# Optimization experiments

Measured on AMD Instinct MI355X. Metric: run time of the kernel, lower is better.

The kernel has to match this reference:

```python
import jax, jax.numpy as jnp
import numpy as np

W_BIT, OUT_F, IN_F, K = 4, 4096, 4096, 16
B, S = 4, 2048


def setup_inputs() -> dict:
    key = jax.random.key(0)
    k1, k2, k3, k4 = jax.random.split(key, 4)
    x = jax.random.normal(k1, (B, S, IN_F), dtype=jnp.float16)
    # bit-packed signs: 8 signs per byte, stored as int32 in [0, 256)
    qweight = jax.random.randint(k2, (W_BIT, OUT_F * IN_F // 8), 0, 256, dtype=jnp.int32)
    u = jax.random.normal(k3, (W_BIT, OUT_F, K), dtype=jnp.float16) * jnp.float16(0.1)
    vt = jax.random.normal(k4, (W_BIT, K, IN_F), dtype=jnp.float16) * jnp.float16(0.1)
    return {"x": x, "qweight": qweight, "u": u, "vt": vt}


def _unpack_sign(qweight, out_f, in_f, dtype):
    # [w_bit, N/8] packed bytes -> [w_bit, out_f, in_f] signs in {-1, +1}
    bits = (qweight[:, :, None] >> jnp.arange(8, dtype=qweight.dtype)) & 1
    sign = (2 * bits - 1).reshape(qweight.shape[0], out_f, in_f)
    return sign.astype(dtype)


def reference(x, qweight, u, vt):
    w_bit, out_f, _ = u.shape
    in_f = vt.shape[2]
    sign = _unpack_sign(qweight, out_f, in_f, u.dtype)          # [w_bit, out, in]
    lowrank = jnp.einsum('bok,bki->boi', u, vt)                  # per-bit u @ vt
    w = jnp.sum(sign * lowrank, axis=0)                          # [out, in]
    return x @ w.T                                               # [B, S, out]
```

## Files before the change

kernel.cpp:

```cpp
#include <hip/hip_runtime.h>
#include <stdint.h>


#define W_BITS 4
#define OUT_F  4096
#define IN_F   4096
#define K_RANK 16
#define M_TOT  8192
#define QW_PER_BIT (OUT_F * IN_F / 8)

typedef __attribute__((ext_vector_type(8))) short bf16x8;
typedef __attribute__((ext_vector_type(4))) float f32x4;

__device__ __forceinline__ unsigned short f2bf(float f) {
  union { float f; unsigned int u; } c; c.f = f;
  unsigned int r = c.u + 0x7fffu + ((c.u >> 16) & 1u);
  return (unsigned short)(r >> 16);
}

__global__ __launch_bounds__(256) void convert_x(
    const float* __restrict__ X, unsigned short* __restrict__ Xb, int n8)
{
  const int stride = gridDim.x * blockDim.x;
  for (int i = blockIdx.x * blockDim.x + threadIdx.x; i < n8; i += stride) {
    const f32x4 a = *reinterpret_cast<const f32x4*>(X + (size_t)i * 8);
    const f32x4 b = *reinterpret_cast<const f32x4*>(X + (size_t)i * 8 + 4);
    unsigned short o8[8] = {f2bf(a[0]), f2bf(a[1]), f2bf(a[2]), f2bf(a[3]),
                            f2bf(b[0]), f2bf(b[1]), f2bf(b[2]), f2bf(b[3])};
    *reinterpret_cast<uint4*>(Xb + (size_t)i * 8) = *reinterpret_cast<const uint4*>(o8);
  }
}

#define TO 4

__global__ __launch_bounds__(256) void build_w(
    const int*   __restrict__ qw,
    const float* __restrict__ u,
    const float* __restrict__ vt,
    unsigned short* __restrict__ w)
{
  const int tid = blockIdx.x * 256 + threadIdx.x;
  const int ig  = tid & 511;
  const int i0  = ig << 3;
  const int ob  = (tid >> 9) << 2;

  float acc[TO][8];
  #pragma unroll
  for (int t = 0; t < TO; ++t)
    #pragma unroll
    for (int ii = 0; ii < 8; ++ii) acc[t][ii] = 0.0f;

  #pragma unroll
  for (int bit = 0; bit < W_BITS; ++bit) {
    float lr[TO][8];
    #pragma unroll
    for (int t = 0; t < TO; ++t)
      #pragma unroll
      for (int ii = 0; ii < 8; ++ii) lr[t][ii] = 0.0f;

    const float* vbase = vt + (size_t)(bit * K_RANK) * IN_F + i0;
    const float* ubase = u + (size_t)(bit * OUT_F + ob) * K_RANK;

    #pragma unroll
    for (int k = 0; k < K_RANK; ++k) {
      const f32x4 v0 = *reinterpret_cast<const f32x4*>(vbase + (size_t)k * IN_F);
      const f32x4 v1 = *reinterpret_cast<const f32x4*>(vbase + (size_t)k * IN_F + 4);
      float vf[8] = {v0[0], v0[1], v0[2], v0[3], v1[0], v1[1], v1[2], v1[3]};
      #pragma unroll
      for (int t = 0; t < TO; ++t) {
        const float uk = ubase[t * K_RANK + k];
        #pragma unroll
        for (int ii = 0; ii < 8; ++ii) lr[t][ii] += uk * vf[ii];
      }
    }

    #pragma unroll
    for (int t = 0; t < TO; ++t) {
      const int q = qw[(size_t)bit * QW_PER_BIT + (size_t)(ob + t) * (IN_F / 8) + ig];
      #pragma unroll
      for (int ii = 0; ii < 8; ++ii)
        acc[t][ii] += ((q >> ii) & 1) ? lr[t][ii] : -lr[t][ii];
    }
  }

  #pragma unroll
  for (int t = 0; t < TO; ++t) {
    unsigned short o8[8];
    #pragma unroll
    for (int ii = 0; ii < 8; ++ii) o8[ii] = f2bf(acc[t][ii]);
    *reinterpret_cast<uint4*>(w + (size_t)(ob + t) * IN_F + i0) =
        *reinterpret_cast<const uint4*>(o8);
  }
}

__device__ __forceinline__ void gll16(unsigned short* lds, const unsigned short* g) {
  __builtin_amdgcn_global_load_lds(
      (const __attribute__((address_space(1))) unsigned int*)g,
      (__attribute__((address_space(3))) unsigned int*)lds,
      16, 0, 0);
}

__global__ __launch_bounds__(512, 2) void gemm_256(
    const unsigned short* __restrict__ X,
    const unsigned short* __restrict__ W,
    float* __restrict__ out)
{
  __shared__ __align__(16) unsigned short Al[2][256][64];
  __shared__ __align__(16) unsigned short Bl[2][256][64];

  const int bid = blockIdx.x;
  const int swz = (bid & 7) * 64 + (bid >> 3);
  const int bm = swz >> 4;
  const int bn = swz & 15;

  const int tid  = threadIdx.x;
  const int lane = tid & 63;
  const int wid  = tid >> 6;
  const int wm   = wid >> 2;
  const int wn   = wid & 3;

  const int sr = tid >> 3;
  const int sc = (((tid & 7) ^ (sr & 7)) << 3);

  const unsigned short* Abase = X + (size_t)(bm * 256 + sr) * IN_F + sc;
  const unsigned short* Bbase = W + (size_t)(bn * 256 + sr) * IN_F + sc;
  unsigned short* Alt = &Al[0][0][0] + tid * 8;
  unsigned short* Blt = &Bl[0][0][0] + tid * 8;

  const int fr  = lane & 15;
  const int sw0 = (((lane >> 4) ^ (fr & 7)) << 3);
  const int aRow = (wm * 16 + fr) * 64;
  const int bRow = (wn * 16 + fr) * 64;
  const unsigned short* Ar = &Al[0][0][0];
  const unsigned short* Br = &Bl[0][0][0];

  f32x4 acc[8][4];
  #pragma unroll
  for (int f = 0; f < 8; ++f)
    #pragma unroll
    for (int g = 0; g < 4; ++g)
      acc[f][g] = (f32x4){0.f, 0.f, 0.f, 0.f};

#define STAGE(buf, h, tn_) do {                                                        \
    const unsigned short* gs_ = ((h) < 2 ? Abase : Bbase)                              \
        + (size_t)(((h) & 1) * 128) * IN_F + (size_t)(tn_) * 64;                       \
    unsigned short* ld_ = ((h) < 2 ? Alt : Blt) + (buf) * 16384 + ((h) & 1) * 8192;    \
    gll16(ld_, gs_);                                                                   \
    gll16(ld_ + 4096, gs_ + (size_t)64 * IN_F);                                        \
  } while (0)

#define WAITBAR() do {                                                                 \
    asm volatile("s_waitcnt vmcnt(4)" ::: "memory");                                   \
    __builtin_amdgcn_s_barrier();                                                      \
    __builtin_amdgcn_sched_barrier(0);                                                 \
  } while (0)

#define LGKMW(n_) do {                                                                 \
    asm volatile("s_waitcnt lgkmcnt(" #n_ ")" ::: "memory");                           \
    __builtin_amdgcn_sched_barrier(0);                                                 \
  } while (0)

#define SB() __builtin_amdgcn_sched_barrier(0)

#define ENDPH() do {                                                                   \
    __builtin_amdgcn_sched_barrier(0);                                                 \
    __builtin_amdgcn_s_barrier();                                                      \
  } while (0)

#define RD_A(base_, mh_, f_, ks_)                                                      \
    aF[f_][ks_] = *reinterpret_cast<const bf16x8*>(                                    \
        Ar + (base_) + ((mh_) * 4 + (f_)) * 2048 + aRow + (((ks_) * 32) ^ sw0))

#define RD_B(dst_, base_, nh_, g_, ks_)                                                \
    dst_[g_][ks_] = *reinterpret_cast<const bf16x8*>(                                  \
        Br + (base_) + ((nh_) * 2 + (g_)) * 4096 + bRow + (((ks_) * 32) ^ sw0))

#define MF(mh_, nh_, f_, g_, ks_, bsrc_)                                               \
    acc[(mh_) * 4 + (f_)][(nh_) * 2 + (g_)] = __builtin_amdgcn_mfma_f32_16x16x32_bf16( \
        aF[f_][ks_], bsrc_[g_][ks_], acc[(mh_) * 4 + (f_)][(nh_) * 2 + (g_)], 0, 0, 0)

#define MF4(mh_, nh_, f_, bsrc_) do {                                                  \
    MF(mh_, nh_, f_, 0, 0, bsrc_); MF(mh_, nh_, f_, 0, 1, bsrc_);                      \
    MF(mh_, nh_, f_, 1, 0, bsrc_); MF(mh_, nh_, f_, 1, 1, bsrc_); } while (0)

#define KTILE(P_, Q_, CC_, OO_, tn_) do {                                              \
    const int cb_ = (CC_) * 16384, ob_ = (OO_) * 16384;                                \
                       \
    STAGE(OO_, 2, tn_);                                                                \
    WAITBAR();                                                                         \
    LGKMW(0);                                                                          \
    __builtin_amdgcn_s_setprio(1);                                                     \
    RD_B(Q_, cb_, 1, 0, 0); SB(); MF4(0, 0, 0, P_); SB();                              \
    RD_B(Q_, cb_, 1, 0, 1); SB(); MF4(0, 0, 1, P_); SB();                              \
    RD_B(Q_, cb_, 1, 1, 0); SB(); MF4(0, 0, 2, P_); SB();                              \
    RD_B(Q_, cb_, 1, 1, 1); SB(); MF4(0, 0, 3, P_);                                    \
    __builtin_amdgcn_s_setprio(0);                                                     \
    ENDPH();                                                                           \
                        \
    STAGE(OO_, 0, tn_);                                                                \
    WAITBAR();                                                                         \
    LGKMW(0);                                                                          \
    __builtin_amdgcn_s_setprio(1);                                                     \
    MF4(0, 1, 0, Q_); SB(); RD_A(cb_, 1, 0, 0); RD_A(cb_, 1, 0, 1); SB();              \
    MF4(0, 1, 1, Q_); SB(); RD_A(cb_, 1, 1, 0); RD_A(cb_, 1, 1, 1); SB();              \
    MF4(0, 1, 2, Q_); SB(); RD_A(cb_, 1, 2, 0); RD_A(cb_, 1, 2, 1); SB();              \
    MF4(0, 1, 3, Q_); SB(); RD_A(cb_, 1, 3, 0); RD_A(cb_, 1, 3, 1);                    \
    __builtin_amdgcn_s_setprio(0);                                                     \
    ENDPH();                                                                           \
                \
    STAGE(OO_, 3, tn_);                                                                \
    WAITBAR();                                                                         \
    LGKMW(0);                                                                          \
    __builtin_amdgcn_s_setprio(1);                                                     \
    MF4(1, 1, 0, Q_); MF4(1, 1, 1, Q_); MF4(1, 1, 2, Q_); MF4(1, 1, 3, Q_);            \
    __builtin_amdgcn_s_setprio(0);                                                     \
    SB();                                                                              \
    RD_B(Q_, ob_, 0, 0, 0); RD_B(Q_, ob_, 0, 0, 1);                                    \
    RD_B(Q_, ob_, 0, 1, 0); RD_B(Q_, ob_, 0, 1, 1);                                    \
    ENDPH();                                                                           \
                  \
    STAGE(OO_, 1, tn_);                                                                \
    WAITBAR();                                                                         \
    LGKMW(4);                                                                          \
    __builtin_amdgcn_s_setprio(1);                                                     \
    MF4(1, 0, 0, P_); SB(); RD_A(ob_, 0, 0, 0); RD_A(ob_, 0, 0, 1); SB();              \
    MF4(1, 0, 1, P_); SB(); RD_A(ob_, 0, 1, 0); RD_A(ob_, 0, 1, 1); SB();              \
    MF4(1, 0, 2, P_); SB(); RD_A(ob_, 0, 2, 0); RD_A(ob_, 0, 2, 1); SB();              \
    MF4(1, 0, 3, P_); SB(); RD_A(ob_, 0, 3, 0); RD_A(ob_, 0, 3, 1);                    \
    __builtin_amdgcn_s_setprio(0);                                                     \
    ENDPH();                                                                           \
  } while (0)

  STAGE(0, 0, 0);
  STAGE(0, 2, 0);
  STAGE(0, 3, 0);
  STAGE(0, 1, 0);
  asm volatile("s_waitcnt vmcnt(4)" ::: "memory");
  __builtin_amdgcn_s_barrier();
  __builtin_amdgcn_sched_barrier(0);

  bf16x8 aF[4][2], bF0[2][2], bF1[2][2];
  RD_A(0, 0, 0, 0); RD_A(0, 0, 0, 1);
  RD_A(0, 0, 1, 0); RD_A(0, 0, 1, 1);
  RD_A(0, 0, 2, 0); RD_A(0, 0, 2, 1);
  RD_A(0, 0, 3, 0); RD_A(0, 0, 3, 1);
  RD_B(bF0, 0, 0, 0, 0); RD_B(bF0, 0, 0, 0, 1);
  RD_B(bF0, 0, 0, 1, 0); RD_B(bF0, 0, 0, 1, 1);

  #pragma unroll 1
  for (int Th = 0; Th < 32; ++Th) {
    const int T0 = 2 * Th;
    const int tnA = T0 + 1;
    const int tnB = (T0 + 2 < 64) ? T0 + 2 : 63;
    KTILE(bF0, bF1, 0, 1, tnA);
    KTILE(bF1, bF0, 1, 0, tnB);
  }

  asm volatile("s_waitcnt vmcnt(0) lgkmcnt(0)" ::: "memory");

  const int rsub = (lane >> 4) << 2;
  #pragma unroll
  for (int f = 0; f < 8; ++f) {
    const int row = bm * 256 + (f * 2 + wm) * 16 + rsub;
    #pragma unroll
    for (int g = 0; g < 4; ++g) {
      const int col = bn * 256 + (g * 4 + wn) * 16 + (lane & 15);
      float* op = out + (size_t)row * OUT_F + col;
      #pragma unroll
      for (int j = 0; j < 4; ++j) op[(size_t)j * OUT_F] = acc[f][g][j];
    }
  }
#undef STAGE
#undef WAITBAR
#undef LGKMW
#undef SB
#undef ENDPH
#undef RD_A
#undef RD_B
#undef MF
#undef MF4
#undef KTILE
}

#define BM 128
#define BN 128
#define BK 32

__device__ __forceinline__ uint4 cvt8(f32x4 a, f32x4 b) {
  unsigned short o8[8] = {f2bf(a[0]), f2bf(a[1]), f2bf(a[2]), f2bf(a[3]),
                          f2bf(b[0]), f2bf(b[1]), f2bf(b[2]), f2bf(b[3])};
  return *reinterpret_cast<const uint4*>(o8);
}

__global__ __launch_bounds__(256) void gemm_f32stage(
    const float* __restrict__ X,
    const unsigned short* __restrict__ W,
    float* __restrict__ out)
{
  __shared__ __align__(16) unsigned short As[BM * BK];
  __shared__ __align__(16) unsigned short Bs[BN * BK];

  const int nbn = OUT_F / BN;
  const int cpx = (M_TOT / BM) * nbn / 8;
  const int bid = blockIdx.x;
  const int swz = (bid & 7) * cpx + (bid >> 3);
  const int bm = swz / nbn;
  const int bn = swz % nbn;

  const int tid  = threadIdx.x;
  const int lane = tid & 63;
  const int wid  = tid >> 6;
  const int wm   = wid >> 1;
  const int wn   = wid & 1;
  const int srow = tid >> 2;
  const int scol = (tid & 3) << 3;

  const float*          Ag = X + (size_t)(bm * BM + srow) * IN_F + scol;
  const unsigned short* Bg = W + (size_t)(bn * BN + srow) * IN_F + scol;

  const int fr = lane & 15;
  const int fk = (lane >> 4) << 3;

  f32x4 acc[4][4];
  #pragma unroll
  for (int m = 0; m < 4; ++m)
    #pragma unroll
    for (int n = 0; n < 4; ++n)
      acc[m][n] = (f32x4){0.f, 0.f, 0.f, 0.f};

  for (int k0 = 0; k0 < IN_F; k0 += BK) {
    const f32x4 a0a = *reinterpret_cast<const f32x4*>(Ag + k0);
    const f32x4 a0b = *reinterpret_cast<const f32x4*>(Ag + k0 + 4);
    const f32x4 a1a = *reinterpret_cast<const f32x4*>(Ag + (size_t)64 * IN_F + k0);
    const f32x4 a1b = *reinterpret_cast<const f32x4*>(Ag + (size_t)64 * IN_F + k0 + 4);
    const uint4 b0  = *reinterpret_cast<const uint4*>(Bg + k0);
    const uint4 b1  = *reinterpret_cast<const uint4*>(Bg + (size_t)64 * IN_F + k0);

    __syncthreads();
    *reinterpret_cast<uint4*>(As + tid * 8)        = cvt8(a0a, a0b);
    *reinterpret_cast<uint4*>(As + 2048 + tid * 8) = cvt8(a1a, a1b);
    *reinterpret_cast<uint4*>(Bs + tid * 8)        = b0;
    *reinterpret_cast<uint4*>(Bs + 2048 + tid * 8) = b1;
    __syncthreads();

    bf16x8 af[4], bfv[4];
    #pragma unroll
    for (int m = 0; m < 4; ++m)
      af[m] = *reinterpret_cast<const bf16x8*>(&As[(wm * 64 + m * 16 + fr) * BK + fk]);
    #pragma unroll
    for (int n = 0; n < 4; ++n)
      bfv[n] = *reinterpret_cast<const bf16x8*>(&Bs[(wn * 64 + n * 16 + fr) * BK + fk]);

    #pragma unroll
    for (int m = 0; m < 4; ++m)
      #pragma unroll
      for (int n = 0; n < 4; ++n)
        acc[m][n] = __builtin_amdgcn_mfma_f32_16x16x32_bf16(af[m], bfv[n], acc[m][n], 0, 0, 0);
  }

  const int rsub = (lane >> 4) << 2;
  #pragma unroll
  for (int m = 0; m < 4; ++m) {
    #pragma unroll
    for (int n = 0; n < 4; ++n) {
      const int col = bn * BN + wn * 64 + n * 16 + (lane & 15);
      #pragma unroll
      for (int j = 0; j < 4; ++j) {
        const int row = bm * BM + wm * 64 + m * 16 + rsub + j;
        out[(size_t)row * OUT_F + col] = acc[m][n][j];
      }
    }
  }
}

extern "C" void kernel_launch(void* const* d_in, const int* in_sizes, int n_in,
                              void* d_out, int out_size, void* d_ws, size_t ws_size,
                              hipStream_t stream) {
  (void)in_sizes; (void)n_in; (void)out_size;

  const float* x  = (const float*)d_in[0];
  const int*   qw = (const int*)d_in[1];
  const float* u  = (const float*)d_in[2];
  const float* vt = (const float*)d_in[3];
  float* out = (float*)d_out;

  unsigned short* w = (unsigned short*)d_ws;
  const size_t W_BYTES  = (size_t)OUT_F * IN_F * 2;
  const size_t XB_BYTES = (size_t)M_TOT * IN_F * 2;

  build_w<<<dim3(2048), dim3(256), 0, stream>>>(qw, u, vt, w);

  if (ws_size >= W_BYTES + XB_BYTES) {
    unsigned short* xb = w + (size_t)OUT_F * IN_F;
    convert_x<<<dim3(2048), dim3(256), 0, stream>>>(x, xb, M_TOT * IN_F / 8);
    gemm_256<<<dim3(512), dim3(512), 0, stream>>>(xb, w, out);
  } else {
    gemm_f32stage<<<dim3(2048), dim3(256), 0, stream>>>(x, w, out);
  }
}
```

Before: 367.6 us.

## Fuse fp32-to-bf16 conversion of X into the pipelined GEMM A-tile staging

Removes the separate convert_x pass and workspace buffer by loading fp32 X tiles into registers inside gemm_256, converting to bf16 and writing them into LDS during later phases, while W still uses direct global-to-LDS loads. This avoids writing and re-reading a bf16 copy of X. In exchange the GEMM reads twice as many bytes for A per tile, uses more registers, and adds conversion ALU work and new wait-count placements in the pipeline. The fallback small-workspace GEMM is deleted.

```diff
diff --git a/kernel.cpp b/kernel.cpp
--- a/kernel.cpp
+++ b/kernel.cpp
@@ -18,17 +18,10 @@
   return (unsigned short)(r >> 16);
 }
 
-__global__ __launch_bounds__(256) void convert_x(
-    const float* __restrict__ X, unsigned short* __restrict__ Xb, int n8)
-{
-  const int stride = gridDim.x * blockDim.x;
-  for (int i = blockIdx.x * blockDim.x + threadIdx.x; i < n8; i += stride) {
-    const f32x4 a = *reinterpret_cast<const f32x4*>(X + (size_t)i * 8);
-    const f32x4 b = *reinterpret_cast<const f32x4*>(X + (size_t)i * 8 + 4);
-    unsigned short o8[8] = {f2bf(a[0]), f2bf(a[1]), f2bf(a[2]), f2bf(a[3]),
-                            f2bf(b[0]), f2bf(b[1]), f2bf(b[2]), f2bf(b[3])};
-    *reinterpret_cast<uint4*>(Xb + (size_t)i * 8) = *reinterpret_cast<const uint4*>(o8);
-  }
+__device__ __forceinline__ uint4 cvt8(f32x4 a, f32x4 b) {
+  unsigned short o8[8] = {f2bf(a[0]), f2bf(a[1]), f2bf(a[2]), f2bf(a[3]),
+                          f2bf(b[0]), f2bf(b[1]), f2bf(b[2]), f2bf(b[3])};
+  return *reinterpret_cast<const uint4*>(o8);
 }
 
 #define TO 4
@@ -101,7 +94,7 @@
 }
 
 __global__ __launch_bounds__(512, 2) void gemm_256(
-    const unsigned short* __restrict__ X,
+    const float* __restrict__ X,
     const unsigned short* __restrict__ W,
     float* __restrict__ out)
 {
@@ -120,10 +113,10 @@
   const int wn   = wid & 3;
 
   const int sr = tid >> 3;
-  const int sc = (((tid & 7) ^ (sr & 7)) << 3);
-
-  const unsigned short* Abase = X + (size_t)(bm * 256 + sr) * IN_F + sc;
-  const unsigned short* Bbase = W + (size_t)(bn * 256 + sr) * IN_F + sc;
+  const int lc = (tid & 7) ^ (sr & 7);
+
+  const float* AgF = X + (size_t)(bm * 256 + sr) * IN_F + lc * 8;
+  const unsigned short* Bbase = W + (size_t)(bn * 256 + sr) * IN_F + lc * 8;
   unsigned short* Alt = &Al[0][0][0] + tid * 8;
   unsigned short* Blt = &Bl[0][0][0] + tid * 8;
 
@@ -141,16 +134,29 @@
     for (int g = 0; g < 4; ++g)
       acc[f][g] = (f32x4){0.f, 0.f, 0.f, 0.f};
 
-#define STAGE(buf, h, tn_) do {                                                        \
-    const unsigned short* gs_ = ((h) < 2 ? Abase : Bbase)                              \
-        + (size_t)(((h) & 1) * 128) * IN_F + (size_t)(tn_) * 64;                       \
-    unsigned short* ld_ = ((h) < 2 ? Alt : Blt) + (buf) * 16384 + ((h) & 1) * 8192;    \
+#define ALOAD(h_, tn_, r0_, r1_, r2_, r3_) do {                                        \
+    const float* g_ = AgF + (size_t)((h_) * 128) * IN_F + (size_t)(tn_) * 64;          \
+    r0_ = *reinterpret_cast<const f32x4*>(g_);                                         \
+    r1_ = *reinterpret_cast<const f32x4*>(g_ + 4);                                     \
+    r2_ = *reinterpret_cast<const f32x4*>(g_ + (size_t)64 * IN_F);                     \
+    r3_ = *reinterpret_cast<const f32x4*>(g_ + (size_t)64 * IN_F + 4);                 \
+  } while (0)
+
+#define AWRITE(buf_, h_, r0_, r1_, r2_, r3_) do {                                      \
+    *reinterpret_cast<uint4*>(Alt + (buf_) * 16384 + (h_) * 8192)        = cvt8(r0_, r1_); \
+    *reinterpret_cast<uint4*>(Alt + (buf_) * 16384 + (h_) * 8192 + 4096) = cvt8(r2_, r3_); \
+  } while (0)
+
+#define BSTAGE(buf_, nh_, tn_) do {                                                    \
+    const unsigned short* gs_ = Bbase + (size_t)((nh_) * 128) * IN_F                   \
+        + (size_t)(tn_) * 64;                                                          \
+    unsigned short* ld_ = Blt + (buf_) * 16384 + (nh_) * 8192;                         \
     gll16(ld_, gs_);                                                                   \
     gll16(ld_ + 4096, gs_ + (size_t)64 * IN_F);                                        \
   } while (0)
 
-#define WAITBAR() do {                                                                 \
-    asm volatile("s_waitcnt vmcnt(4)" ::: "memory");                                   \
+#define WAITBARN(n_) do {                                                              \
+    asm volatile("s_waitcnt vmcnt(" #n_ ")" ::: "memory");                             \
     __builtin_amdgcn_s_barrier();                                                      \
     __builtin_amdgcn_sched_barrier(0);                                                 \
   } while (0)
@@ -185,9 +191,10 @@
 
 #define KTILE(P_, Q_, CC_, OO_, tn_) do {                                              \
     const int cb_ = (CC_) * 16384, ob_ = (OO_) * 16384;                                \
-                       \
-    STAGE(OO_, 2, tn_);                                                                \
-    WAITBAR();                                                                         \
+               \
+    ALOAD(0, tn_, a0r0, a0r1, a0r2, a0r3);                                             \
+    BSTAGE(OO_, 0, tn_);                                                               \
+    WAITBARN(6);                                                                       \
     LGKMW(0);                                                                          \
     __builtin_amdgcn_s_setprio(1);                                                     \
     RD_B(Q_, cb_, 1, 0, 0); SB(); MF4(0, 0, 0, P_); SB();                              \
@@ -196,9 +203,10 @@
     RD_B(Q_, cb_, 1, 1, 1); SB(); MF4(0, 0, 3, P_);                                    \
     __builtin_amdgcn_s_setprio(0);                                                     \
     ENDPH();                                                                           \
-                        \
-    STAGE(OO_, 0, tn_);                                                                \
-    WAITBAR();                                                                         \
+              \
+    ALOAD(1, tn_, a1r0, a1r1, a1r2, a1r3);                                             \
+    BSTAGE(OO_, 1, tn_);                                                               \
+    WAITBARN(6);                                                                       \
     LGKMW(0);                                                                          \
     __builtin_amdgcn_s_setprio(1);                                                     \
     MF4(0, 1, 0, Q_); SB(); RD_A(cb_, 1, 0, 0); RD_A(cb_, 1, 0, 1); SB();              \
@@ -207,43 +215,50 @@
     MF4(0, 1, 3, Q_); SB(); RD_A(cb_, 1, 3, 0); RD_A(cb_, 1, 3, 1);                    \
     __builtin_amdgcn_s_setprio(0);                                                     \
     ENDPH();                                                                           \
-                \
-    STAGE(OO_, 3, tn_);                                                                \
-    WAITBAR();                                                                         \
+             \
+    WAITBARN(6);                                                                       \
     LGKMW(0);                                                                          \
     __builtin_amdgcn_s_setprio(1);                                                     \
     MF4(1, 1, 0, Q_); MF4(1, 1, 1, Q_); MF4(1, 1, 2, Q_); MF4(1, 1, 3, Q_);            \
     __builtin_amdgcn_s_setprio(0);                                                     \
     SB();                                                                              \
+    AWRITE(OO_, 0, a0r0, a0r1, a0r2, a0r3);                                            \
+    SB();                                                                              \
     RD_B(Q_, ob_, 0, 0, 0); RD_B(Q_, ob_, 0, 0, 1);                                    \
     RD_B(Q_, ob_, 0, 1, 0); RD_B(Q_, ob_, 0, 1, 1);                                    \
+    LGKMW(4);                                                                          \
     ENDPH();                                                                           \
-                  \
-    STAGE(OO_, 1, tn_);                                                                \
-    WAITBAR();                                                                         \
+            \
+    WAITBARN(2);                                                                       \
     LGKMW(4);                                                                          \
     __builtin_amdgcn_s_setprio(1);                                                     \
-    MF4(1, 0, 0, P_); SB(); RD_A(ob_, 0, 0, 0); RD_A(ob_, 0, 0, 1); SB();              \
-    MF4(1, 0, 1, P_); SB(); RD_A(ob_, 0, 1, 0); RD_A(ob_, 0, 1, 1); SB();              \
-    MF4(1, 0, 2, P_); SB(); RD_A(ob_, 0, 2, 0); RD_A(ob_, 0, 2, 1); SB();              \
-    MF4(1, 0, 3, P_); SB(); RD_A(ob_, 0, 3, 0); RD_A(ob_, 0, 3, 1);                    \
+    MF4(1, 0, 0, P_); MF4(1, 0, 1, P_); MF4(1, 0, 2, P_); MF4(1, 0, 3, P_);            \
     __builtin_amdgcn_s_setprio(0);                                                     \
+    SB();                                                                              \
+    AWRITE(OO_, 1, a1r0, a1r1, a1r2, a1r3);                                            \
+    SB();                                                                              \
+    RD_A(ob_, 0, 0, 0); RD_A(ob_, 0, 0, 1); RD_A(ob_, 0, 1, 0); RD_A(ob_, 0, 1, 1);    \
+    RD_A(ob_, 0, 2, 0); RD_A(ob_, 0, 2, 1); RD_A(ob_, 0, 3, 0); RD_A(ob_, 0, 3, 1);    \
+    LGKMW(8);                                                                          \
     ENDPH();                                                                           \
   } while (0)
 
-  STAGE(0, 0, 0);
-  STAGE(0, 2, 0);
-  STAGE(0, 3, 0);
-  STAGE(0, 1, 0);
+  bf16x8 aF[4][2], bF0[2][2], bF1[2][2];
+  f32x4 a0r0, a0r1, a0r2, a0r3, a1r0, a1r1, a1r2, a1r3;
+
+  ALOAD(0, 0, a0r0, a0r1, a0r2, a0r3);
+  ALOAD(1, 0, a1r0, a1r1, a1r2, a1r3);
+  BSTAGE(0, 0, 0);
+  BSTAGE(0, 1, 0);
   asm volatile("s_waitcnt vmcnt(4)" ::: "memory");
+  __builtin_amdgcn_sched_barrier(0);
+  AWRITE(0, 0, a0r0, a0r1, a0r2, a0r3);
+  AWRITE(0, 1, a1r0, a1r1, a1r2, a1r3);
+  asm volatile("s_waitcnt vmcnt(0) lgkmcnt(0)" ::: "memory");
   __builtin_amdgcn_s_barrier();
   __builtin_amdgcn_sched_barrier(0);
-
-  bf16x8 aF[4][2], bF0[2][2], bF1[2][2];
-  RD_A(0, 0, 0, 0); RD_A(0, 0, 0, 1);
-  RD_A(0, 0, 1, 0); RD_A(0, 0, 1, 1);
-  RD_A(0, 0, 2, 0); RD_A(0, 0, 2, 1);
-  RD_A(0, 0, 3, 0); RD_A(0, 0, 3, 1);
+  RD_A(0, 0, 0, 0); RD_A(0, 0, 0, 1); RD_A(0, 0, 1, 0); RD_A(0, 0, 1, 1);
+  RD_A(0, 0, 2, 0); RD_A(0, 0, 2, 1); RD_A(0, 0, 3, 0); RD_A(0, 0, 3, 1);
   RD_B(bF0, 0, 0, 0, 0); RD_B(bF0, 0, 0, 0, 1);
   RD_B(bF0, 0, 0, 1, 0); RD_B(bF0, 0, 0, 1, 1);
 
@@ -270,8 +285,10 @@
       for (int j = 0; j < 4; ++j) op[(size_t)j * OUT_F] = acc[f][g][j];
     }
   }
-#undef STAGE
-#undef WAITBAR
+#undef ALOAD
+#undef AWRITE
+#undef BSTAGE
+#undef WAITBARN
 #undef LGKMW
 #undef SB
 #undef ENDPH
@@ -282,101 +299,10 @@
 #undef KTILE
 }
 
-#define BM 128
-#define BN 128
-#define BK 32
-
-__device__ __forceinline__ uint4 cvt8(f32x4 a, f32x4 b) {
-  unsigned short o8[8] = {f2bf(a[0]), f2bf(a[1]), f2bf(a[2]), f2bf(a[3]),
-                          f2bf(b[0]), f2bf(b[1]), f2bf(b[2]), f2bf(b[3])};
-  return *reinterpret_cast<const uint4*>(o8);
-}
-
-__global__ __launch_bounds__(256) void gemm_f32stage(
-    const float* __restrict__ X,
-    const unsigned short* __restrict__ W,
-    float* __restrict__ out)
-{
-  __shared__ __align__(16) unsigned short As[BM * BK];
-  __shared__ __align__(16) unsigned short Bs[BN * BK];
-
-  const int nbn = OUT_F / BN;
-  const int cpx = (M_TOT / BM) * nbn / 8;
-  const int bid = blockIdx.x;
-  const int swz = (bid & 7) * cpx + (bid >> 3);
-  const int bm = swz / nbn;
-  const int bn = swz % nbn;
-
-  const int tid  = threadIdx.x;
-  const int lane = tid & 63;
-  const int wid  = tid >> 6;
-  const int wm   = wid >> 1;
-  const int wn   = wid & 1;
-  const int srow = tid >> 2;
-  const int scol = (tid & 3) << 3;
-
-  const float*          Ag = X + (size_t)(bm * BM + srow) * IN_F + scol;
-  const unsigned short* Bg = W + (size_t)(bn * BN + srow) * IN_F + scol;
-
-  const int fr = lane & 15;
-  const int fk = (lane >> 4) << 3;
-
-  f32x4 acc[4][4];
-  #pragma unroll
-  for (int m = 0; m < 4; ++m)
-    #pragma unroll
-    for (int n = 0; n < 4; ++n)
-      acc[m][n] = (f32x4){0.f, 0.f, 0.f, 0.f};
-
-  for (int k0 = 0; k0 < IN_F; k0 += BK) {
-    const f32x4 a0a = *reinterpret_cast<const f32x4*>(Ag + k0);
-    const f32x4 a0b = *reinterpret_cast<const f32x4*>(Ag + k0 + 4);
-    const f32x4 a1a = *reinterpret_cast<const f32x4*>(Ag + (size_t)64 * IN_F + k0);
-    const f32x4 a1b = *reinterpret_cast<const f32x4*>(Ag + (size_t)64 * IN_F + k0 + 4);
-    const uint4 b0  = *reinterpret_cast<const uint4*>(Bg + k0);
-    const uint4 b1  = *reinterpret_cast<const uint4*>(Bg + (size_t)64 * IN_F + k0);
-
-    __syncthreads();
-    *reinterpret_cast<uint4*>(As + tid * 8)        = cvt8(a0a, a0b);
-    *reinterpret_cast<uint4*>(As + 2048 + tid * 8) = cvt8(a1a, a1b);
-    *reinterpret_cast<uint4*>(Bs + tid * 8)        = b0;
-    *reinterpret_cast<uint4*>(Bs + 2048 + tid * 8) = b1;
-    __syncthreads();
-
-    bf16x8 af[4], bfv[4];
-    #pragma unroll
-    for (int m = 0; m < 4; ++m)
-      af[m] = *reinterpret_cast<const bf16x8*>(&As[(wm * 64 + m * 16 + fr) * BK + fk]);
-    #pragma unroll
-    for (int n = 0; n < 4; ++n)
-      bfv[n] = *reinterpret_cast<const bf16x8*>(&Bs[(wn * 64 + n * 16 + fr) * BK + fk]);
-
-    #pragma unroll
-    for (int m = 0; m < 4; ++m)
-      #pragma unroll
-      for (int n = 0; n < 4; ++n)
-        acc[m][n] = __builtin_amdgcn_mfma_f32_16x16x32_bf16(af[m], bfv[n], acc[m][n], 0, 0, 0);
-  }
-
-  const int rsub = (lane >> 4) << 2;
-  #pragma unroll
-  for (int m = 0; m < 4; ++m) {
-    #pragma unroll
-    for (int n = 0; n < 4; ++n) {
-      const int col = bn * BN + wn * 64 + n * 16 + (lane & 15);
-      #pragma unroll
-      for (int j = 0; j < 4; ++j) {
-        const int row = bm * BM + wm * 64 + m * 16 + rsub + j;
-        out[(size_t)row * OUT_F + col] = acc[m][n][j];
-      }
-    }
-  }
-}
-
 extern "C" void kernel_launch(void* const* d_in, const int* in_sizes, int n_in,
                               void* d_out, int out_size, void* d_ws, size_t ws_size,
                               hipStream_t stream) {
-  (void)in_sizes; (void)n_in; (void)out_size;
+  (void)in_sizes; (void)n_in; (void)out_size; (void)ws_size;
 
   const float* x  = (const float*)d_in[0];
   const int*   qw = (const int*)d_in[1];
@@ -385,16 +311,7 @@
   float* out = (float*)d_out;
 
   unsigned short* w = (unsigned short*)d_ws;
-  const size_t W_BYTES  = (size_t)OUT_F * IN_F * 2;
-  const size_t XB_BYTES = (size_t)M_TOT * IN_F * 2;
 
   build_w<<<dim3(2048), dim3(256), 0, stream>>>(qw, u, vt, w);
-
-  if (ws_size >= W_BYTES + XB_BYTES) {
-    unsigned short* xb = w + (size_t)OUT_F * IN_F;
-    convert_x<<<dim3(2048), dim3(256), 0, stream>>>(x, xb, M_TOT * IN_F / 8);
-    gemm_256<<<dim3(512), dim3(512), 0, stream>>>(xb, w, out);
-  } else {
-    gemm_f32stage<<<dim3(2048), dim3(256), 0, stream>>>(x, w, out);
-  }
-}
+  gemm_256<<<dim3(512), dim3(512), 0, stream>>>(x, w, out);
+}
```

After: 504.6 us. 1.37x slower.
